# Kernel tuning notes

Measured on AMD Instinct MI355X. Metric: run time of the kernel, lower is better.

## Reference

```python
import jax, jax.numpy as jnp
import numpy as np

T = 32          # chain length (init arg)
K = 2048        # particles per timestep (Ks)
RES = 0.5       # observed scalar (init buffer)
LIKE_STD = 1.0  # likelihood std (init arg)
LOG2PI = float(np.log(2.0 * np.pi))


def _logpdf(x, mu, std):
    # Normal(mu, std).log_prob(x)
    z = (x - mu) / std
    return -0.5 * z * z - jnp.log(std) - 0.5 * LOG2PI


def logmmmeanexp(X, Y):
    # log( exp(X) @ exp(Y) / X.shape[1] ), numerically stabilized exactly as the torch code
    x = jnp.max(X, axis=1, keepdims=True)
    y = jnp.max(Y, axis=0, keepdims=True)
    return x + y + jnp.log(jnp.exp(X - x) @ jnp.exp(Y - y)) - jnp.log(jnp.asarray(X.shape[1], X.dtype))


def setup_inputs() -> dict:
    key = jax.random.key(0)
    eps = jax.random.normal(key, (T, K), dtype=jnp.float32)
    means = jnp.zeros((T,), jnp.float32)
    # matches the torch init: sqrt((1+arange(T))/T)
    log_stds = jnp.sqrt((1.0 + jnp.arange(T, dtype=jnp.float32)) / T)
    return {"means": means, "log_stds": log_stds, "eps": eps}


def reference(means, log_stds, eps):
    std = jnp.exp(log_stds)                            # proposal stds, (T,)
    zs = means[:, None] + std[:, None] * eps           # reparameterized samples, (T,K)
    log_q = _logpdf(zs, means[:, None], std[:, None])  # proposal log-probs, (T,K)
    sp = jnp.sqrt(1.0 / T)                             # prior/transition std

    # first factor: prior over z_0 minus proposal, (1,K)
    r0 = (_logpdf(zs[0], 0.0, sp) - log_q[0])[None, :]
    # middle factors: transition log-probs, (T-1, K, K); Ms[i][j,k] = logN(zs[i+1,k]; zs[i,j], sp) - log_q[i+1,k]
    Ms = _logpdf(zs[1:, None, :], zs[:-1, :, None], sp) - log_q[1:, None, :]

    def step(r, M):
        return logmmmeanexp(r, M), None

    r, _ = jax.lax.scan(step, r0, Ms)
    # likelihood factor, (K,1)
    L = _logpdf(jnp.float32(RES), zs[-1][:, None], jnp.float32(LIKE_STD))
    return logmmmeanexp(r, L)  # (1,1) log marginal-likelihood estimate
```

## Files before the change

### kernel.cpp

```cpp
#include <hip/hip_runtime.h>
#include <math.h>

#define T 32
#define K 2048
#define NBLOCKS 256
#define NTHREADS 512
#define HB 128
#define CPB 16
#define QS 4
#define SSTRIDE 32
#define L2E_F 1.4426950408889634f
#define LN2_F 0.6931471805599453f
#define LOG2PI_F 1.8378770664093453f
#define SP_F     0.17677669529663687f
#define LOG_SP_F (-1.7328679513998633f)
#define CNORM_F  (-(LOG_SP_F) - 0.5f * LOG2PI_F)

#if __has_builtin(__builtin_amdgcn_exp2f)
#define EXP2F(x) __builtin_amdgcn_exp2f(x)
#else
#define EXP2F(x) exp2f(x)
#endif
#if __has_builtin(__builtin_amdgcn_logf)
#define LOG2F(x) __builtin_amdgcn_logf(x)
#else
#define LOG2F(x) log2f(x)
#endif

__device__ __forceinline__ float aload4(const float* p) {
    return __hip_atomic_load(p, __ATOMIC_RELAXED, __HIP_MEMORY_SCOPE_AGENT);
}
__device__ __forceinline__ void astore4(float* p, float v) {
    __hip_atomic_store(p, v, __ATOMIC_RELAXED, __HIP_MEMORY_SCOPE_AGENT);
}
__device__ __forceinline__ int sload(const int* p) {
    return __hip_atomic_load(p, __ATOMIC_RELAXED, __HIP_MEMORY_SCOPE_AGENT);
}
__device__ __forceinline__ void sstore(int* p, int v) {
    __hip_atomic_store(p, v, __ATOMIC_RELAXED, __HIP_MEMORY_SCOPE_AGENT);
}

__global__ __launch_bounds__(NTHREADS) void fused_kernel(
    const float* __restrict__ means, const float* __restrict__ log_stds,
    const float* __restrict__ eps, float* __restrict__ fbuf,
    float* __restrict__ bbuf, int* __restrict__ fsent, int* __restrict__ bsent,
    float* __restrict__ out)
{
    __shared__ float2 shzD[2][K];
    __shared__ float2 lzc[T][CPB];
    __shared__ float smu[T], sstd[T], slq2[T];
    __shared__ float red[NTHREADS];
    __shared__ int ldsflag;

    const int tid  = threadIdx.x;
    const int b    = blockIdx.x;
    const bool fwd = (b < HB);
    const int lb   = fwd ? b : b - HB;
    const int col0 = lb * CPB;

    if (tid == 0) ldsflag = 0;

    {
        int t = tid >> 4, dcol = tid & 15;
        float mu = means[t];
        float st = expf(log_stds[t]);
        if (dcol == 0) {
            smu[t] = mu; sstd[t] = st;
            slq2[t] = L2E_F * (logf(st) + 0.5f * LOG2PI_F);
        }
        float e = eps[t * K + col0 + dcol];
        float z = fmaf(st, e, mu);
        float log_q = fmaf(-0.5f * e, e, -logf(st) - 0.5f * LOG2PI_F);
        float tz2 = (32.0f * L2E_F) * z;
        if (fwd) {
            float cm2 = fmaf((-16.0f * L2E_F) * z, z,
                             L2E_F * (CNORM_F - log_q)) - 11.0f;
            lzc[t][dcol] = make_float2(tz2, cm2);
            if (t == 0) {
                float r0 = fmaf(-16.0f * z, z, CNORM_F) - log_q;
                astore4(&fbuf[col0 + dcol], r0 * L2E_F);
            }
        } else {
            float cm2 = fmaf((-16.0f * L2E_F) * z, z, L2E_F * CNORM_F) - 11.0f;
            lzc[t][dcol] = make_float2(tz2, cm2);
            if (t == T - 1) {
                float d = 0.5f - z;
                float c31 = fmaf(-0.5f * d, d, -0.5f * LOG2PI_F);
                astore4(&bbuf[col0 + dcol], c31 * L2E_F);
            }
        }
    }
    __syncthreads();
    int* mysent = fwd ? fsent : bsent;
    if (tid == 0) sstore(&mysent[lb * SSTRIDE], 1);

    const int lane = tid & 63;
    const int wave = tid >> 6;
    float* mybuf = fwd ? fbuf : bbuf;
    const int nstep = fwd ? 16 : 15;

    for (int p = 0; p < nstep; ++p) {
        const int par  = p & 1;
        const int need = p + 1;
        const int tin  = fwd ? p : 31 - p;
        const int town = fwd ? p + 1 : 30 - p;
        const float mu_i  = smu[tin];
        const float std_i = sstd[tin];
        const float lqc   = slq2[tin];
        const float* erow = eps + tin * K;

        float zloc[QS], dadd[QS];
        #pragma unroll
        for (int q = 0; q < QS; ++q) {
            float e = erow[tid + q * NTHREADS];
            float z = fmaf(std_i, e, mu_i);
            zloc[q] = z;
            float base = fwd ? 0.0f : fmaf((0.5f * L2E_F) * e, e, lqc);
            dadd[q] = fmaf((-16.0f * L2E_F) * z, z, base);
        }

        if (wave == 0) {
            const int* s0 = mysent + lane * SSTRIDE;
            const int* s1 = mysent + (lane + 64) * SSTRIDE;
            for (;;) {
                int v0 = sload(s0);
                int v1 = sload(s1);
                if (__all(min(v0, v1) >= need)) break;
                __builtin_amdgcn_s_sleep(1);
            }
            __hip_atomic_store(&ldsflag, need, __ATOMIC_RELEASE,
                               __HIP_MEMORY_SCOPE_WORKGROUP);
        } else {
            while (__hip_atomic_load(&ldsflag, __ATOMIC_ACQUIRE,
                                     __HIP_MEMORY_SCOPE_WORKGROUP) < need)
                __builtin_amdgcn_s_sleep(1);
        }

        const float* mrow = mybuf + par * K;
        float rv[QS];
        #pragma unroll
        for (int q = 0; q < QS; ++q) rv[q] = aload4(&mrow[tid + q * NTHREADS]);
        #pragma unroll
        for (int q = 0; q < QS; ++q)
            shzD[par][tid + q * NTHREADS] = make_float2(zloc[q], rv[q] + dadd[q]);
        __syncthreads();

        const float4* shp = (const float4*)&shzD[par][0];
        float2 zcA = lzc[town][2 * wave];
        float2 zcB = lzc[town][2 * wave + 1];
        float4 fr[16];
        #pragma unroll
        for (int i = 0; i < 16; ++i) fr[i] = shp[lane + (i << 6)];
        float m0 = -INFINITY, m1 = -INFINITY;
        #pragma unroll
        for (int i = 0; i < 16; ++i) {
            m0 = fmaxf(m0, fmaxf(fmaf(zcA.x, fr[i].x, fr[i].y),
                                 fmaf(zcA.x, fr[i].z, fr[i].w)));
            m1 = fmaxf(m1, fmaxf(fmaf(zcB.x, fr[i].x, fr[i].y),
                                 fmaf(zcB.x, fr[i].z, fr[i].w)));
        }
        #pragma unroll
        for (int off = 32; off >= 1; off >>= 1) {
            m0 = fmaxf(m0, __shfl_xor(m0, off, 64));
            m1 = fmaxf(m1, __shfl_xor(m1, off, 64));
        }
        float s0 = 0.0f, s1 = 0.0f;
        #pragma unroll
        for (int i = 0; i < 16; ++i) {
            s0 += EXP2F(fmaf(zcA.x, fr[i].x, fr[i].y) - m0);
            s0 += EXP2F(fmaf(zcA.x, fr[i].z, fr[i].w) - m0);
            s1 += EXP2F(fmaf(zcB.x, fr[i].x, fr[i].y) - m1);
            s1 += EXP2F(fmaf(zcB.x, fr[i].z, fr[i].w) - m1);
        }
        #pragma unroll
        for (int off = 32; off >= 1; off >>= 1) {
            s0 += __shfl_xor(s0, off, 64);
            s1 += __shfl_xor(s1, off, 64);
        }
        if (lane < 2) {
            float mm = lane ? m1 : m0;
            float sv = lane ? s1 : s0;
            float cm = lane ? zcB.y : zcA.y;
            astore4(&mybuf[(par ^ 1) * K + col0 + 2 * wave + lane],
                    cm + mm + LOG2F(sv));
        }
        __syncthreads();
        if (tid == 0) sstore(&mysent[lb * SSTRIDE], p + 2);
    }

    if (b == 0) {
        for (;;) {
            int f0 = sload(&fsent[lane * SSTRIDE]);
            int f1 = sload(&fsent[(lane + 64) * SSTRIDE]);
            int g0 = sload(&bsent[lane * SSTRIDE]);
            int g1 = sload(&bsent[(lane + 64) * SSTRIDE]);
            bool ok = (min(f0, f1) >= 17) && (min(g0, g1) >= 16);
            if (__all(ok)) break;
            __builtin_amdgcn_s_sleep(1);
        }
        float vals[QS];
        float m = -INFINITY;
        #pragma unroll
        for (int q = 0; q < QS; ++q) {
            int j = tid + q * NTHREADS;
            float v = aload4(&fbuf[j]) + aload4(&bbuf[K + j]);
            vals[q] = v;
            m = fmaxf(m, v);
        }
        red[tid] = m; __syncthreads();
        for (int off = NTHREADS / 2; off >= 1; off >>= 1) {
            if (tid < off) red[tid] = fmaxf(red[tid], red[tid + off]);
            __syncthreads();
        }
        m = red[0]; __syncthreads();
        float ssum = 0.0f;
        #pragma unroll
        for (int q = 0; q < QS; ++q) ssum += EXP2F(vals[q] - m);
        red[tid] = ssum; __syncthreads();
        for (int off = NTHREADS / 2; off >= 1; off >>= 1) {
            if (tid < off) red[tid] += red[tid + off];
            __syncthreads();
        }
        if (tid == 0) out[0] = LN2_F * (m + LOG2F(red[0]) - 11.0f);
    }
}

extern "C" void kernel_launch(void* const* d_in, const int* in_sizes, int n_in,
                              void* d_out, int out_size, void* d_ws, size_t ws_size,
                              hipStream_t stream) {
    const float* means    = (const float*)d_in[0];
    const float* log_stds = (const float*)d_in[1];
    const float* eps      = (const float*)d_in[2];
    float* out = (float*)d_out;

    float* fbuf = (float*)d_ws;
    float* bbuf = fbuf + 2 * K;
    int*   fsent = (int*)(bbuf + 2 * K);
    int*   bsent = fsent + 128 * SSTRIDE;

    fused_kernel<<<NBLOCKS, NTHREADS, 0, stream>>>(
        means, log_stds, eps, fbuf, bbuf, fsent, bsent, out);
}
```

Measured before the change: 113.9 us.

## Distribute final meet-in-middle step across all blocks and streamline polling

Drops the forward chain from 16 to 15 steps, so both halves take the same number of steps. The last transition (15→16) is now computed in a distributed way: every block evaluates 8 rows of the forward-backward junction against the backward vector. Block 0 then does a small final logsumexp over 256 per-block partials, replacing the former single-block 2048-element reduction. It also caches per-lane readiness flags in the spin loops and packs the two per-wave outputs into one 64-bit atomic store, at the cost of an extra grid-wide barrier round.

```diff
diff --git a/kernel.cpp b/kernel.cpp
--- a/kernel.cpp
+++ b/kernel.cpp
@@ -9,6 +9,7 @@
 #define CPB 16
 #define QS 4
 #define SSTRIDE 32
+#define NSTEP 15
 #define L2E_F 1.4426950408889634f
 #define LN2_F 0.6931471805599453f
 #define LOG2PI_F 1.8378770664093453f
@@ -32,6 +33,12 @@
 }
 __device__ __forceinline__ void astore4(float* p, float v) {
     __hip_atomic_store(p, v, __ATOMIC_RELAXED, __HIP_MEMORY_SCOPE_AGENT);
+}
+__device__ __forceinline__ void astore8(float* p, float a, float b) {
+    union { float2 f; unsigned long long u; } v;
+    v.f = make_float2(a, b);
+    __hip_atomic_store((unsigned long long*)p, v.u, __ATOMIC_RELAXED,
+                       __HIP_MEMORY_SCOPE_AGENT);
 }
 __device__ __forceinline__ int sload(const int* p) {
     return __hip_atomic_load(p, __ATOMIC_RELAXED, __HIP_MEMORY_SCOPE_AGENT);
@@ -97,9 +104,8 @@
     const int lane = tid & 63;
     const int wave = tid >> 6;
     float* mybuf = fwd ? fbuf : bbuf;
-    const int nstep = fwd ? 16 : 15;
-
-    for (int p = 0; p < nstep; ++p) {
+
+    for (int p = 0; p < NSTEP; ++p) {
         const int par  = p & 1;
         const int need = p + 1;
         const int tin  = fwd ? p : 31 - p;
@@ -122,10 +128,11 @@
         if (wave == 0) {
             const int* s0 = mysent + lane * SSTRIDE;
             const int* s1 = mysent + (lane + 64) * SSTRIDE;
+            bool ok0 = false, ok1 = false;
             for (;;) {
-                int v0 = sload(s0);
-                int v1 = sload(s1);
-                if (__all(min(v0, v1) >= need)) break;
+                if (!ok0) ok0 = sload(s0) >= need;
+                if (!ok1) ok1 = sload(s1) >= need;
+                if (__all(ok0 & ok1)) break;
                 __builtin_amdgcn_s_sleep(1);
             }
             __hip_atomic_store(&ldsflag, need, __ATOMIC_RELEASE,
@@ -177,51 +184,117 @@
             s0 += __shfl_xor(s0, off, 64);
             s1 += __shfl_xor(s1, off, 64);
         }
-        if (lane < 2) {
-            float mm = lane ? m1 : m0;
-            float sv = lane ? s1 : s0;
-            float cm = lane ? zcB.y : zcA.y;
-            astore4(&mybuf[(par ^ 1) * K + col0 + 2 * wave + lane],
-                    cm + mm + LOG2F(sv));
+        if (lane == 0) {
+            astore8(&mybuf[(par ^ 1) * K + col0 + 2 * wave],
+                    zcA.y + m0 + LOG2F(s0), zcB.y + m1 + LOG2F(s1));
         }
         __syncthreads();
         if (tid == 0) sstore(&mysent[lb * SSTRIDE], p + 2);
     }
 
-    if (b == 0) {
+    if (wave == 0) {
+        const int* f0 = fsent + lane * SSTRIDE;
+        const int* f1 = fsent + (lane + 64) * SSTRIDE;
+        const int* g0 = bsent + lane * SSTRIDE;
+        const int* g1 = bsent + (lane + 64) * SSTRIDE;
+        bool a0 = false, a1 = false, a2 = false, a3 = false;
         for (;;) {
-            int f0 = sload(&fsent[lane * SSTRIDE]);
-            int f1 = sload(&fsent[(lane + 64) * SSTRIDE]);
-            int g0 = sload(&bsent[lane * SSTRIDE]);
-            int g1 = sload(&bsent[(lane + 64) * SSTRIDE]);
-            bool ok = (min(f0, f1) >= 17) && (min(g0, g1) >= 16);
-            if (__all(ok)) break;
+            if (!a0) a0 = sload(f0) >= 16;
+            if (!a1) a1 = sload(f1) >= 16;
+            if (!a2) a2 = sload(g0) >= 16;
+            if (!a3) a3 = sload(g1) >= 16;
+            if (__all(a0 & a1 & a2 & a3)) break;
             __builtin_amdgcn_s_sleep(1);
         }
-        float vals[QS];
+        __hip_atomic_store(&ldsflag, 16, __ATOMIC_RELEASE,
+                           __HIP_MEMORY_SCOPE_WORKGROUP);
+    } else {
+        while (__hip_atomic_load(&ldsflag, __ATOMIC_ACQUIRE,
+                                 __HIP_MEMORY_SCOPE_WORKGROUP) < 16)
+            __builtin_amdgcn_s_sleep(1);
+    }
+
+    {
+        const float mu16 = smu[16], st16 = sstd[16];
+        const float lqc16 = slq2[16] + L2E_F * CNORM_F;
+        #pragma unroll
+        for (int q = 0; q < QS; ++q) {
+            int k = tid + q * NTHREADS;
+            float e = eps[16 * K + k];
+            float z = fmaf(st16, e, mu16);
+            float bk = aload4(&bbuf[K + k]) +
+                       fmaf((-16.0f * L2E_F) * z, z,
+                            fmaf((0.5f * L2E_F) * e, e, lqc16));
+            shzD[0][k] = make_float2((32.0f * L2E_F) * z, bk);
+        }
+    }
+    __syncthreads();
+
+    {
+        const int j = b * 8 + wave;
+        float e15 = eps[15 * K + j];
+        float zj = fmaf(sstd[15], e15, smu[15]);
+        float cj = fmaf((-16.0f * L2E_F) * zj, zj, aload4(&fbuf[K + j]));
+        const float4* shp = (const float4*)&shzD[0][0];
+        float4 fr[16];
+        #pragma unroll
+        for (int i = 0; i < 16; ++i) fr[i] = shp[lane + (i << 6)];
         float m = -INFINITY;
         #pragma unroll
-        for (int q = 0; q < QS; ++q) {
-            int j = tid + q * NTHREADS;
-            float v = aload4(&fbuf[j]) + aload4(&bbuf[K + j]);
-            vals[q] = v;
-            m = fmaxf(m, v);
-        }
-        red[tid] = m; __syncthreads();
-        for (int off = NTHREADS / 2; off >= 1; off >>= 1) {
-            if (tid < off) red[tid] = fmaxf(red[tid], red[tid + off]);
-            __syncthreads();
-        }
-        m = red[0]; __syncthreads();
-        float ssum = 0.0f;
-        #pragma unroll
-        for (int q = 0; q < QS; ++q) ssum += EXP2F(vals[q] - m);
-        red[tid] = ssum; __syncthreads();
-        for (int off = NTHREADS / 2; off >= 1; off >>= 1) {
-            if (tid < off) red[tid] += red[tid + off];
-            __syncthreads();
-        }
-        if (tid == 0) out[0] = LN2_F * (m + LOG2F(red[0]) - 11.0f);
+        for (int i = 0; i < 16; ++i)
+            m = fmaxf(m, fmaxf(fmaf(fr[i].x, zj, fr[i].y),
+                               fmaf(fr[i].z, zj, fr[i].w)));
+        #pragma unroll
+        for (int off = 32; off >= 1; off >>= 1) m = fmaxf(m, __shfl_xor(m, off, 64));
+        float s = 0.0f;
+        #pragma unroll
+        for (int i = 0; i < 16; ++i) {
+            s += EXP2F(fmaf(fr[i].x, zj, fr[i].y) - m);
+            s += EXP2F(fmaf(fr[i].z, zj, fr[i].w) - m);
+        }
+        #pragma unroll
+        for (int off = 32; off >= 1; off >>= 1) s += __shfl_xor(s, off, 64);
+        if (lane == 0) red[wave] = cj + m + LOG2F(s);
+    }
+    __syncthreads();
+
+    if (tid == 0) {
+        float m8 = -INFINITY;
+        #pragma unroll
+        for (int i = 0; i < 8; ++i) m8 = fmaxf(m8, red[i]);
+        float s8 = 0.0f;
+        #pragma unroll
+        for (int i = 0; i < 8; ++i) s8 += EXP2F(red[i] - m8);
+        astore4(&fbuf[b], m8 + LOG2F(s8));
+    }
+    __syncthreads();
+    if (tid == 0) sstore(&mysent[lb * SSTRIDE], 17);
+
+    if (b == 0 && wave == 0) {
+        const int* f0 = fsent + lane * SSTRIDE;
+        const int* f1 = fsent + (lane + 64) * SSTRIDE;
+        const int* g0 = bsent + lane * SSTRIDE;
+        const int* g1 = bsent + (lane + 64) * SSTRIDE;
+        bool a0 = false, a1 = false, a2 = false, a3 = false;
+        for (;;) {
+            if (!a0) a0 = sload(f0) >= 17;
+            if (!a1) a1 = sload(f1) >= 17;
+            if (!a2) a2 = sload(g0) >= 17;
+            if (!a3) a3 = sload(g1) >= 17;
+            if (__all(a0 & a1 & a2 & a3)) break;
+            __builtin_amdgcn_s_sleep(1);
+        }
+        float v0 = aload4(&fbuf[lane]);
+        float v1 = aload4(&fbuf[lane + 64]);
+        float v2 = aload4(&fbuf[lane + 128]);
+        float v3 = aload4(&fbuf[lane + 192]);
+        float m = fmaxf(fmaxf(v0, v1), fmaxf(v2, v3));
+        #pragma unroll
+        for (int off = 32; off >= 1; off >>= 1) m = fmaxf(m, __shfl_xor(m, off, 64));
+        float s = EXP2F(v0 - m) + EXP2F(v1 - m) + EXP2F(v2 - m) + EXP2F(v3 - m);
+        #pragma unroll
+        for (int off = 32; off >= 1; off >>= 1) s += __shfl_xor(s, off, 64);
+        if (lane == 0) out[0] = LN2_F * (m + LOG2F(s) - 22.0f);
     }
 }
 
```

New measurement: 114.3 us. No clear change (+0.3%).
